# Kernel optimization log

Measured on AMD Instinct MI355X. Metric: run time of the kernel, lower is better.

Reference implementation:

```python
import jax, jax.numpy as jnp
import numpy as np

B, S, IN, E, H, NH = 32, 1024, 16, 128, 256, 4
DH = E // NH
EPS = 1e-5


def _ln(x, g, b):
    mu = jnp.mean(x, axis=-1, keepdims=True)
    var = jnp.mean(jnp.square(x - mu), axis=-1, keepdims=True)
    return (x - mu) * jax.lax.rsqrt(var + EPS) * g + b


def setup_inputs() -> dict:
    key = jax.random.key(0)
    ks = iter(jax.random.split(key, 32))
    n = lambda shape, s=0.02: jax.random.normal(next(ks), shape, jnp.float32) * s
    inp = {
        "x": jax.random.normal(next(ks), (B, S, IN), jnp.float32),
        "mask": jax.random.uniform(next(ks), (B, S), jnp.float32),
        "embed_w": n((E, IN)), "embed_b": jnp.zeros((E,), jnp.float32),
        # 3 encoder layers, params stacked on leading layer axis
        "in_proj_w": n((3, 3 * E, E)), "in_proj_b": jnp.zeros((3, 3 * E), jnp.float32),
        "out_w": n((3, E, E)), "out_b": jnp.zeros((3, E), jnp.float32),
        "ln1_g": jnp.ones((3, E), jnp.float32), "ln1_b": jnp.zeros((3, E), jnp.float32),
        "ln2_g": jnp.ones((3, E), jnp.float32), "ln2_b": jnp.zeros((3, E), jnp.float32),
        "ffn_w1": n((3, E, E)), "ffn_b1": jnp.zeros((3, E), jnp.float32),
        "ffn_w2": n((3, E, E)), "ffn_b2": jnp.zeros((3, E), jnp.float32),
        "cls_w1": n((H, E)), "cls_b1": jnp.zeros((H,), jnp.float32),
        "cls_w2": n((H, H)), "cls_b2": jnp.zeros((H,), jnp.float32),
        "cls_w3": n((H, H)), "cls_b3": jnp.zeros((H,), jnp.float32),
        "cls_w4": n((1, H)), "cls_b4": jnp.zeros((1,), jnp.float32),
    }
    return inp


def _encoder_layer(x, ipw, ipb, ow, ob, g1, b1, g2, b2, w1, fb1, w2, fb2):
    # PyTorch TransformerEncoderLayer, norm_first=False (post-norm), relu FFN
    qkv = x @ ipw.T + ipb                      # [B,S,3E]
    q, k, v = jnp.split(qkv, 3, axis=-1)
    q = q.reshape(B, S, NH, DH).transpose(0, 2, 1, 3)
    k = k.reshape(B, S, NH, DH).transpose(0, 2, 1, 3)
    v = v.reshape(B, S, NH, DH).transpose(0, 2, 1, 3)
    scores = jnp.einsum("bhqd,bhkd->bhqk", q, k) / np.sqrt(DH)  # naive O(S^2) math SDPA
    attn = jax.nn.softmax(scores, axis=-1)
    o = jnp.einsum("bhqk,bhkd->bhqd", attn, v)
    o = o.transpose(0, 2, 1, 3).reshape(B, S, E) @ ow.T + ob
    x = _ln(x + o, g1, b1)
    ff = jax.nn.relu(x @ w1.T + fb1) @ w2.T + fb2
    return _ln(x + ff, g2, b2)


def reference(x, mask, embed_w, embed_b, in_proj_w, in_proj_b, out_w, out_b,
              ln1_g, ln1_b, ln2_g, ln2_b, ffn_w1, ffn_b1, ffn_w2, ffn_b2,
              cls_w1, cls_b1, cls_w2, cls_b2, cls_w3, cls_b3, cls_w4, cls_b4):
    h = jax.nn.relu(x @ embed_w.T + embed_b)   # [B,S,E]
    for i in range(3):
        h = _encoder_layer(h, in_proj_w[i], in_proj_b[i], out_w[i], out_b[i],
                           ln1_g[i], ln1_b[i], ln2_g[i], ln2_b[i],
                           ffn_w1[i], ffn_b1[i], ffn_w2[i], ffn_b2[i])
    pooled = jnp.sum(h * mask[:, :, None], axis=1)  # [B,E] masked sum pool
    z = jax.nn.relu(pooled @ cls_w1.T + cls_b1)
    z = jax.nn.relu(z @ cls_w2.T + cls_b2)
    z = jax.nn.relu(z @ cls_w3.T + cls_b3)
    return jax.nn.sigmoid(z @ cls_w4.T + cls_b4)    # [B,1]
```

## Files before the change

kernel.cpp:

```cpp
#include <hip/hip_runtime.h>
#include <hip/hip_bf16.h>
#include <math.h>

#define B 32
#define S 1024
#define IN_DIM 16
#define E 128
#define NH 4
#define DH 32
#define HDIM 256
#define ROWS (B*S)
#define EPS 1e-5f

#define N_IPW (3*384*128)
#define N_SQ  (3*128*128)
#define NCVT ((N_IPW + 3*N_SQ) / 256)

typedef __bf16 bf16x8 __attribute__((ext_vector_type(8)));
typedef __bf16 bf16x4 __attribute__((ext_vector_type(4)));
typedef __bf16 bf16x2 __attribute__((ext_vector_type(2)));
typedef float f32x4 __attribute__((ext_vector_type(4)));

union BF2U { bf16x2 b; unsigned int u; };
__device__ inline unsigned int pk2(float a, float b) {
    BF2U x; x.b[0] = (__bf16)a; x.b[1] = (__bf16)b; return x.u;
}

union U8 { bf16x8 v8; bf16x4 v4[2]; };
__device__ inline void st8(__bf16* p, bf16x8 v) {
    U8 u; u.v8 = v;
    *(bf16x4*)p = u.v4[0];
    *(bf16x4*)(p + 4) = u.v4[1];
}
__device__ inline bf16x8 ld8(const __bf16* p) {
    U8 u;
    u.v4[0] = *(const bf16x4*)p;
    u.v4[1] = *(const bf16x4*)(p + 4);
    return u.v8;
}

__global__ __launch_bounds__(256) void k_embedcvt(
        const float* __restrict__ ipw, const float* __restrict__ ow,
        const float* __restrict__ w1, const float* __restrict__ w2,
        __bf16* __restrict__ wbo,
        const float* __restrict__ x, const float* __restrict__ W,
        const float* __restrict__ bias, __bf16* __restrict__ hb)
{
    int t = threadIdx.x;
    if (blockIdx.x < NCVT) {
        int i = blockIdx.x * 256 + t;
        float v;
        if (i < N_IPW) v = ipw[i];
        else if (i < N_IPW + N_SQ) v = ow[i - N_IPW];
        else if (i < N_IPW + 2 * N_SQ) v = w1[i - N_IPW - N_SQ];
        else v = w2[i - N_IPW - 2 * N_SQ];
        wbo[i] = (__bf16)v;
        return;
    }
    int row0 = (blockIdx.x - NCVT) * 16;
    __shared__ float xs[16][16];
    xs[t >> 4][t & 15] = x[(row0 + (t >> 4)) * IN_DIM + (t & 15)];
    __syncthreads();
    int sub = t >> 7, tc = t & 127;
    float w[16];
#pragma unroll
    for (int i = 0; i < 16; ++i) w[i] = W[tc * 16 + i];
    float bb = bias[tc];
#pragma unroll
    for (int rr = 0; rr < 8; ++rr) {
        int lr = sub * 8 + rr;
        float acc = bb;
#pragma unroll
        for (int i = 0; i < 16; ++i) acc += xs[lr][i] * w[i];
        hb[(size_t)(row0 + lr) * E + tc] = (__bf16)fmaxf(acc, 0.f);
    }
}

__global__ __launch_bounds__(256) void k_gemm_qkv(const __bf16* __restrict__ A,
        const __bf16* __restrict__ W, const float* __restrict__ bias,
        __bf16* __restrict__ qk, __bf16* __restrict__ vt)
{
    __shared__ __attribute__((aligned(16))) __bf16 As[128][132];
    __shared__ __attribute__((aligned(16))) __bf16 Ws[64][132];
    int t = threadIdx.x;
    int m0 = blockIdx.y * 128, n0 = blockIdx.x * 64;
    {
        int arow = t >> 1, acol = (t & 1) * 64;
        const __bf16* Ap = A + (size_t)(m0 + arow) * 128 + acol;
#pragma unroll
        for (int j = 0; j < 8; ++j)
            st8(&As[arow][acol + j * 8], *(const bf16x8*)&Ap[j * 8]);
        int wrow = t >> 2, wcol = (t & 3) * 32;
        const __bf16* Wp = W + (size_t)(n0 + wrow) * 128 + wcol;
#pragma unroll
        for (int j = 0; j < 4; ++j)
            st8(&Ws[wrow][wcol + j * 8], *(const bf16x8*)&Wp[j * 8]);
    }
    __syncthreads();
    int lane = t & 63, wv = t >> 6;
    int l15 = lane & 15, quad = lane >> 4;
    int wm = (wv & 1) * 64, wn = (wv >> 1) * 32;
    f32x4 acc[2][4];
#pragma unroll
    for (int i = 0; i < 2; ++i)
#pragma unroll
        for (int j = 0; j < 4; ++j) acc[i][j] = (f32x4){0.f, 0.f, 0.f, 0.f};
#pragma unroll
    for (int kc = 0; kc < 4; ++kc) {
        bf16x8 aw[2], ba[4];
#pragma unroll
        for (int nc = 0; nc < 2; ++nc)
            aw[nc] = ld8(&Ws[wn + nc * 16 + l15][kc * 32 + quad * 8]);
#pragma unroll
        for (int mc = 0; mc < 4; ++mc)
            ba[mc] = ld8(&As[wm + mc * 16 + l15][kc * 32 + quad * 8]);
#pragma unroll
        for (int nc = 0; nc < 2; ++nc)
#pragma unroll
            for (int mc = 0; mc < 4; ++mc)
                acc[nc][mc] = __builtin_amdgcn_mfma_f32_16x16x32_bf16(aw[nc], ba[mc], acc[nc][mc], 0, 0, 0);
    }
#pragma unroll
    for (int nc = 0; nc < 2; ++nc) {
        float4 bv = *(const float4*)&bias[n0 + wn + nc * 16 + quad * 4];
#pragma unroll
        for (int mc = 0; mc < 4; ++mc) {
            float v0 = acc[nc][mc][0] + bv.x;
            float v1 = acc[nc][mc][1] + bv.y;
            float v2 = acc[nc][mc][2] + bv.z;
            float v3 = acc[nc][mc][3] + bv.w;
            int n = n0 + wn + nc * 16 + quad * 4;
            int m = m0 + wm + mc * 16 + l15;
            if (n < 256) {
                uint2 u; u.x = pk2(v0, v1); u.y = pk2(v2, v3);
                *(uint2*)&qk[(size_t)m * 256 + n] = u;
            } else {
                int dp = n - 256;
                int hq = dp >> 5, d0 = dp & 31;
                __bf16* vp = vt + (((size_t)(m >> 10) * 4 + hq) * 32 + d0) * 1024 + (m & 1023);
                vp[0] = (__bf16)v0; vp[1024] = (__bf16)v1;
                vp[2048] = (__bf16)v2; vp[3072] = (__bf16)v3;
            }
        }
    }
}

__global__ __launch_bounds__(256) void k_attn4(const __bf16* __restrict__ qk,
        const __bf16* __restrict__ vt, __bf16* __restrict__ O)
{
    int qt = blockIdx.x & 7, bh = blockIdx.x >> 3;
    int hh = bh & 3, b = bh >> 2;
    __shared__ __attribute__((aligned(16))) __bf16 Kb[2][64][36];
    __shared__ __attribute__((aligned(16))) __bf16 Vb[2][32][68];
    __shared__ __attribute__((aligned(16))) __bf16 Pm[2][4][16][68];
    int t = threadIdx.x, lane = t & 63, wv = t >> 6;
    int l15 = lane & 15, quad = lane >> 4;
    const __bf16* qbase = qk + (size_t)(b * S) * 256 + hh * 32;
    const __bf16* kbase = qk + (size_t)(b * S) * 256 + 128 + hh * 32;
    const __bf16* vbase = vt + ((size_t)(b * 4 + hh) * 32) * 1024;
    const float qscale = 0.1767766952966369f * 1.4426950408889634f * 8388608.0f;
    const float C2 = 1065101558.0f;
    const f32x4 cinit = {C2, C2, C2, C2};
    bf16x8 vones;
#pragma unroll
    for (int j = 0; j < 8; ++j) vones[j] = (__bf16)1.0f;

    bf16x8 bQ[2];
#pragma unroll
    for (int gq = 0; gq < 2; ++gq) {
        bf16x8 qv = *(const bf16x8*)&qbase[(size_t)(qt * 128 + gq * 64 + wv * 16 + l15) * 256 + quad * 8];
#pragma unroll
        for (int j = 0; j < 8; ++j) bQ[gq][j] = (__bf16)((float)qv[j] * qscale);
    }

    int ksr = t >> 2, ksc = (t & 3) * 8;
    int vsr = t >> 3, vsc = (t & 7) * 8;

    {
        bf16x8 k0 = *(const bf16x8*)&kbase[(size_t)ksr * 256 + ksc];
        bf16x8 v0 = *(const bf16x8*)&vbase[(size_t)vsr * 1024 + vsc];
        st8(&Kb[0][ksr][ksc], k0);
        st8(&Vb[0][vsr][vsc], v0);
    }
    __syncthreads();

    f32x4 o[2][2], ol[2];
#pragma unroll
    for (int gq = 0; gq < 2; ++gq) {
        ol[gq] = (f32x4){0.f, 0.f, 0.f, 0.f};
#pragma unroll
        for (int j = 0; j < 2; ++j) o[gq][j] = (f32x4){0.f, 0.f, 0.f, 0.f};
    }

    for (int it = 0; it < 16; ++it) {
        const int cur = it & 1;
        bf16x8 knext, vnext;
        if (it < 15) {
            knext = *(const bf16x8*)&kbase[(size_t)((it + 1) * 64 + ksr) * 256 + ksc];
            vnext = *(const bf16x8*)&vbase[(size_t)vsr * 1024 + (it + 1) * 64 + vsc];
        }
        bf16x8 aK[4];
#pragma unroll
        for (int c = 0; c < 4; ++c)
            aK[c] = ld8(&Kb[cur][c * 16 + l15][quad * 8]);
        bf16x8 bv[2][2];
#pragma unroll
        for (int kc = 0; kc < 2; ++kc) {
            bv[kc][0] = ld8(&Vb[cur][l15][kc * 32 + quad * 8]);
            bv[kc][1] = ld8(&Vb[cur][16 + l15][kc * 32 + quad * 8]);
        }
#pragma unroll
        for (int gq = 0; gq < 2; ++gq) {
            f32x4 sf[4];
#pragma unroll
            for (int c = 0; c < 4; ++c)
                sf[c] = __builtin_amdgcn_mfma_f32_16x16x32_bf16(aK[c], bQ[gq], cinit, 0, 0, 0);
#pragma unroll
            for (int c = 0; c < 4; ++c) {
                int i0 = (int)sf[c][0];
                int i1 = (int)sf[c][1];
                int i2 = (int)sf[c][2];
                int i3 = (int)sf[c][3];
                uint2 u;
                u.x = __builtin_amdgcn_perm((unsigned)i1, (unsigned)i0, 0x07060302u);
                u.y = __builtin_amdgcn_perm((unsigned)i3, (unsigned)i2, 0x07060302u);
                *(uint2*)&Pm[gq][wv][l15][c * 16 + quad * 4] = u;
            }
        }
        __asm__ __volatile__("" ::: "memory");
#pragma unroll
        for (int gq = 0; gq < 2; ++gq) {
#pragma unroll
            for (int kc = 0; kc < 2; ++kc) {
                bf16x8 ap = ld8(&Pm[gq][wv][l15][kc * 32 + quad * 8]);
                o[gq][0] = __builtin_amdgcn_mfma_f32_16x16x32_bf16(ap, bv[kc][0], o[gq][0], 0, 0, 0);
                o[gq][1] = __builtin_amdgcn_mfma_f32_16x16x32_bf16(ap, bv[kc][1], o[gq][1], 0, 0, 0);
                ol[gq]   = __builtin_amdgcn_mfma_f32_16x16x32_bf16(ap, vones, ol[gq], 0, 0, 0);
            }
        }
        __asm__ __volatile__("" ::: "memory");
        if (it < 15) {
            st8(&Kb[cur ^ 1][ksr][ksc], knext);
            st8(&Vb[cur ^ 1][vsr][vsc], vnext);
            __syncthreads();
        }
    }

#pragma unroll
    for (int gq = 0; gq < 2; ++gq) {
#pragma unroll
        for (int reg = 0; reg < 4; ++reg) {
            float linv = 1.f / ol[gq][reg];
            int row = qt * 128 + gq * 64 + wv * 16 + quad * 4 + reg;
            __bf16* op = O + ((size_t)(b * S) + row) * E + hh * 32;
            op[l15] = (__bf16)(o[gq][0][reg] * linv);
            op[16 + l15] = (__bf16)(o[gq][1][reg] * linv);
        }
    }
}

__global__ __launch_bounds__(256) void k_layer2(const __bf16* __restrict__ t0b,
        const __bf16* __restrict__ Wo, const float* __restrict__ ob,
        const float* __restrict__ g1, const float* __restrict__ bt1,
        const __bf16* __restrict__ W1, const float* __restrict__ b1v,
        const __bf16* __restrict__ W2, const float* __restrict__ b2v,
        const float* __restrict__ g2, const float* __restrict__ bt2,
        __bf16* __restrict__ hb)
{
    __shared__ __attribute__((aligned(16))) __bf16 As[64][132];
    __shared__ __attribute__((aligned(16))) __bf16 Ws[128][132];
    __shared__ float red[2][64][2];
    int t = threadIdx.x;
    int m0 = blockIdx.x * 64;
    int arow = t >> 2, acol = (t & 3) * 32;
    int wrow = t >> 1, wcol = (t & 1) * 64;
    {
        const __bf16* Ap = t0b + (size_t)(m0 + arow) * 128 + acol;
#pragma unroll
        for (int j = 0; j < 4; ++j)
            st8(&As[arow][acol + j * 8], *(const bf16x8*)&Ap[j * 8]);
        const __bf16* Wp = Wo + (size_t)wrow * 128 + wcol;
#pragma unroll
        for (int j = 0; j < 8; ++j)
            st8(&Ws[wrow][wcol + j * 8], *(const bf16x8*)&Wp[j * 8]);
    }
    __syncthreads();
    int lane = t & 63, wv = t >> 6;
    int l15 = lane & 15, quad = lane >> 4;
    int nh = wv & 1, mh = wv >> 1;
    f32x4 acc[4][2];

#pragma unroll
    for (int i = 0; i < 4; ++i)
#pragma unroll
        for (int j = 0; j < 2; ++j) acc[i][j] = (f32x4){0.f, 0.f, 0.f, 0.f};
#pragma unroll
    for (int kc = 0; kc < 4; ++kc) {
        bf16x8 aw[4], ba[2];
#pragma unroll
        for (int nc = 0; nc < 4; ++nc)
            aw[nc] = ld8(&Ws[nh * 64 + nc * 16 + l15][kc * 32 + quad * 8]);
#pragma unroll
        for (int mc = 0; mc < 2; ++mc)
            ba[mc] = ld8(&As[mh * 32 + mc * 16 + l15][kc * 32 + quad * 8]);
#pragma unroll
        for (int nc = 0; nc < 4; ++nc)
#pragma unroll
            for (int mc = 0; mc < 2; ++mc)
                acc[nc][mc] = __builtin_amdgcn_mfma_f32_16x16x32_bf16(aw[nc], ba[mc], acc[nc][mc], 0, 0, 0);
    }
    float s1[2] = {0.f, 0.f}, s2[2] = {0.f, 0.f};
#pragma unroll
    for (int nc = 0; nc < 4; ++nc) {
        float4 bv = *(const float4*)&ob[nh * 64 + nc * 16 + quad * 4];
#pragma unroll
        for (int mc = 0; mc < 2; ++mc) {
            int m = m0 + mh * 32 + mc * 16 + l15;
            bf16x4 rv = *(const bf16x4*)&hb[(size_t)m * 128 + nh * 64 + nc * 16 + quad * 4];
            acc[nc][mc][0] += bv.x + (float)rv[0];
            acc[nc][mc][1] += bv.y + (float)rv[1];
            acc[nc][mc][2] += bv.z + (float)rv[2];
            acc[nc][mc][3] += bv.w + (float)rv[3];
#pragma unroll
            for (int i = 0; i < 4; ++i) {
                s1[mc] += acc[nc][mc][i];
                s2[mc] += acc[nc][mc][i] * acc[nc][mc][i];
            }
        }
    }
#pragma unroll
    for (int mc = 0; mc < 2; ++mc) {
        s1[mc] += __shfl_xor(s1[mc], 16); s1[mc] += __shfl_xor(s1[mc], 32);
        s2[mc] += __shfl_xor(s2[mc], 16); s2[mc] += __shfl_xor(s2[mc], 32);
    }
    if (quad == 0) {
#pragma unroll
        for (int mc = 0; mc < 2; ++mc) {
            red[nh][mh * 32 + mc * 16 + l15][0] = s1[mc];
            red[nh][mh * 32 + mc * 16 + l15][1] = s2[mc];
        }
    }
    __syncthreads();
    float mu[2], rs[2];
#pragma unroll
    for (int mc = 0; mc < 2; ++mc) {
        int r = mh * 32 + mc * 16 + l15;
        float S1 = red[0][r][0] + red[1][r][0];
        float S2 = red[0][r][1] + red[1][r][1];
        mu[mc] = S1 * (1.f / 128.f);
        float var = S2 * (1.f / 128.f) - mu[mc] * mu[mc];
        rs[mc] = rsqrtf(var + EPS);
    }
    bf16x4 res2[4][2];
#pragma unroll
    for (int nc = 0; nc < 4; ++nc) {
        float4 gv = *(const float4*)&g1[nh * 64 + nc * 16 + quad * 4];
        float4 bb = *(const float4*)&bt1[nh * 64 + nc * 16 + quad * 4];
#pragma unroll
        for (int mc = 0; mc < 2; ++mc) {
            float o0 = (acc[nc][mc][0] - mu[mc]) * rs[mc] * gv.x + bb.x;
            float o1 = (acc[nc][mc][1] - mu[mc]) * rs[mc] * gv.y + bb.y;
            float o2 = (acc[nc][mc][2] - mu[mc]) * rs[mc] * gv.z + bb.z;
            float o3 = (acc[nc][mc][3] - mu[mc]) * rs[mc] * gv.w + bb.w;
            bf16x4 xb;
            xb[0] = (__bf16)o0; xb[1] = (__bf16)o1;
            xb[2] = (__bf16)o2; xb[3] = (__bf16)o3;
            res2[nc][mc] = xb;
            *(bf16x4*)&As[mh * 32 + mc * 16 + l15][nh * 64 + nc * 16 + quad * 4] = xb;
        }
    }
    {
        const __bf16* Wp = W1 + (size_t)wrow * 128 + wcol;
#pragma unroll
        for (int j = 0; j < 8; ++j)
            st8(&Ws[wrow][wcol + j * 8], *(const bf16x8*)&Wp[j * 8]);
    }
    __syncthreads();

#pragma unroll
    for (int i = 0; i < 4; ++i)
#pragma unroll
        for (int j = 0; j < 2; ++j) acc[i][j] = (f32x4){0.f, 0.f, 0.f, 0.f};
#pragma unroll
    for (int kc = 0; kc < 4; ++kc) {
        bf16x8 aw[4], ba[2];
#pragma unroll
        for (int nc = 0; nc < 4; ++nc)
            aw[nc] = ld8(&Ws[nh * 64 + nc * 16 + l15][kc * 32 + quad * 8]);
#pragma unroll
        for (int mc = 0; mc < 2; ++mc)
            ba[mc] = ld8(&As[mh * 32 + mc * 16 + l15][kc * 32 + quad * 8]);
#pragma unroll
        for (int nc = 0; nc < 4; ++nc)
#pragma unroll
            for (int mc = 0; mc < 2; ++mc)
                acc[nc][mc] = __builtin_amdgcn_mfma_f32_16x16x32_bf16(aw[nc], ba[mc], acc[nc][mc], 0, 0, 0);
    }
    __syncthreads();
#pragma unroll
    for (int nc = 0; nc < 4; ++nc) {
        float4 bv = *(const float4*)&b1v[nh * 64 + nc * 16 + quad * 4];
#pragma unroll
        for (int mc = 0; mc < 2; ++mc) {
            float v0 = fmaxf(acc[nc][mc][0] + bv.x, 0.f);
            float v1 = fmaxf(acc[nc][mc][1] + bv.y, 0.f);
            float v2 = fmaxf(acc[nc][mc][2] + bv.z, 0.f);
            float v3 = fmaxf(acc[nc][mc][3] + bv.w, 0.f);
            uint2 u; u.x = pk2(v0, v1); u.y = pk2(v2, v3);
            *(uint2*)&As[mh * 32 + mc * 16 + l15][nh * 64 + nc * 16 + quad * 4] = u;
        }
    }
    {
        const __bf16* Wp = W2 + (size_t)wrow * 128 + wcol;
#pragma unroll
        for (int j = 0; j < 8; ++j)
            st8(&Ws[wrow][wcol + j * 8], *(const bf16x8*)&Wp[j * 8]);
    }
    __syncthreads();

#pragma unroll
    for (int i = 0; i < 4; ++i)
#pragma unroll
        for (int j = 0; j < 2; ++j) acc[i][j] = (f32x4){0.f, 0.f, 0.f, 0.f};
#pragma unroll
    for (int kc = 0; kc < 4; ++kc) {
        bf16x8 aw[4], ba[2];
#pragma unroll
        for (int nc = 0; nc < 4; ++nc)
            aw[nc] = ld8(&Ws[nh * 64 + nc * 16 + l15][kc * 32 + quad * 8]);
#pragma unroll
        for (int mc = 0; mc < 2; ++mc)
            ba[mc] = ld8(&As[mh * 32 + mc * 16 + l15][kc * 32 + quad * 8]);
#pragma unroll
        for (int nc = 0; nc < 4; ++nc)
#pragma unroll
            for (int mc = 0; mc < 2; ++mc)
                acc[nc][mc] = __builtin_amdgcn_mfma_f32_16x16x32_bf16(aw[nc], ba[mc], acc[nc][mc], 0, 0, 0);
    }
    s1[0] = s1[1] = s2[0] = s2[1] = 0.f;
#pragma unroll
    for (int nc = 0; nc < 4; ++nc) {
        float4 bv = *(const float4*)&b2v[nh * 64 + nc * 16 + quad * 4];
#pragma unroll
        for (int mc = 0; mc < 2; ++mc) {
            acc[nc][mc][0] += bv.x + (float)res2[nc][mc][0];
            acc[nc][mc][1] += bv.y + (float)res2[nc][mc][1];
            acc[nc][mc][2] += bv.z + (float)res2[nc][mc][2];
            acc[nc][mc][3] += bv.w + (float)res2[nc][mc][3];
#pragma unroll
            for (int i = 0; i < 4; ++i) {
                s1[mc] += acc[nc][mc][i];
                s2[mc] += acc[nc][mc][i] * acc[nc][mc][i];
            }
        }
    }
#pragma unroll
    for (int mc = 0; mc < 2; ++mc) {
        s1[mc] += __shfl_xor(s1[mc], 16); s1[mc] += __shfl_xor(s1[mc], 32);
        s2[mc] += __shfl_xor(s2[mc], 16); s2[mc] += __shfl_xor(s2[mc], 32);
    }
    if (quad == 0) {
#pragma unroll
        for (int mc = 0; mc < 2; ++mc) {
            red[nh][mh * 32 + mc * 16 + l15][0] = s1[mc];
            red[nh][mh * 32 + mc * 16 + l15][1] = s2[mc];
        }
    }
    __syncthreads();
#pragma unroll
    for (int mc = 0; mc < 2; ++mc) {
        int r = mh * 32 + mc * 16 + l15;
        float S1 = red[0][r][0] + red[1][r][0];
        float S2 = red[0][r][1] + red[1][r][1];
        mu[mc] = S1 * (1.f / 128.f);
        float var = S2 * (1.f / 128.f) - mu[mc] * mu[mc];
        rs[mc] = rsqrtf(var + EPS);
    }
#pragma unroll
    for (int nc = 0; nc < 4; ++nc) {
        float4 gv = *(const float4*)&g2[nh * 64 + nc * 16 + quad * 4];
        float4 bb = *(const float4*)&bt2[nh * 64 + nc * 16 + quad * 4];
#pragma unroll
        for (int mc = 0; mc < 2; ++mc) {
            int m = m0 + mh * 32 + mc * 16 + l15;
            float o0 = (acc[nc][mc][0] - mu[mc]) * rs[mc] * gv.x + bb.x;
            float o1 = (acc[nc][mc][1] - mu[mc]) * rs[mc] * gv.y + bb.y;
            float o2 = (acc[nc][mc][2] - mu[mc]) * rs[mc] * gv.z + bb.z;
            float o3 = (acc[nc][mc][3] - mu[mc]) * rs[mc] * gv.w + bb.w;
            uint2 u; u.x = pk2(o0, o1); u.y = pk2(o2, o3);
            *(uint2*)&hb[(size_t)m * 128 + nh * 64 + nc * 16 + quad * 4] = u;
        }
    }
}

__global__ __launch_bounds__(128) void k_pool1(const __bf16* __restrict__ h,
        const float* __restrict__ mask, float* __restrict__ part)
{
    int bx = blockIdx.x;
    int b = bx >> 3, ch = bx & 7, t = threadIdx.x;
    float acc = 0.f;
    const __bf16* hp = h + (size_t)(b * S + ch * 128) * E + t;
    const float* mp = mask + b * S + ch * 128;
    for (int s = 0; s < 128; ++s) acc += (float)hp[(size_t)s * E] * mp[s];
    part[(size_t)bx * E + t] = acc;
}

__global__ __launch_bounds__(256) void k_head(const float* __restrict__ part,
        const float* __restrict__ cw1, const float* __restrict__ cb1,
        const float* __restrict__ cw2, const float* __restrict__ cb2,
        const float* __restrict__ cw3, const float* __restrict__ cb3,
        const float* __restrict__ cw4, const float* __restrict__ cb4,
        float* __restrict__ out)
{
    int b = blockIdx.x, t = threadIdx.x;
    __shared__ float p[128], za[256], zb[256];
    __shared__ float red4[4];
    if (t < 128) {
        float a = 0.f;
#pragma unroll
        for (int c = 0; c < 8; ++c) a += part[(size_t)(b * 8 + c) * 128 + t];
        p[t] = a;
    }
    __syncthreads();
    float a1 = cb1[t];
    for (int k = 0; k < 128; ++k) a1 += p[k] * cw1[t * 128 + k];
    za[t] = fmaxf(a1, 0.f);
    __syncthreads();
    float a2 = cb2[t];
    for (int k = 0; k < 256; ++k) a2 += za[k] * cw2[t * 256 + k];
    zb[t] = fmaxf(a2, 0.f);
    __syncthreads();
    float a3 = cb3[t];
    for (int k = 0; k < 256; ++k) a3 += zb[k] * cw3[t * 256 + k];
    float z3 = fmaxf(a3, 0.f);
    float prt = z3 * cw4[t];
#pragma unroll
    for (int o2 = 32; o2; o2 >>= 1) prt += __shfl_xor(prt, o2);
    if ((t & 63) == 0) red4[t >> 6] = prt;
    __syncthreads();
    if (t == 0) {
        float sum = red4[0] + red4[1] + red4[2] + red4[3] + cb4[0];
        out[b] = 1.f / (1.f + __expf(-sum));
    }
}

extern "C" void kernel_launch(void* const* d_in, const int* in_sizes, int n_in,
                              void* d_out, int out_size, void* d_ws, size_t ws_size,
                              hipStream_t stream)
{
    const float* x     = (const float*)d_in[0];
    const float* mask  = (const float*)d_in[1];
    const float* emb_w = (const float*)d_in[2];
    const float* emb_b = (const float*)d_in[3];
    const float* ipw   = (const float*)d_in[4];
    const float* ipb   = (const float*)d_in[5];
    const float* ow    = (const float*)d_in[6];
    const float* ob    = (const float*)d_in[7];
    const float* ln1g  = (const float*)d_in[8];
    const float* ln1b  = (const float*)d_in[9];
    const float* ln2g  = (const float*)d_in[10];
    const float* ln2b  = (const float*)d_in[11];
    const float* w1    = (const float*)d_in[12];
    const float* fb1   = (const float*)d_in[13];
    const float* w2    = (const float*)d_in[14];
    const float* fb2   = (const float*)d_in[15];
    const float* cw1   = (const float*)d_in[16];
    const float* cb1   = (const float*)d_in[17];
    const float* cw2   = (const float*)d_in[18];
    const float* cb2   = (const float*)d_in[19];
    const float* cw3   = (const float*)d_in[20];
    const float* cb3   = (const float*)d_in[21];
    const float* cw4   = (const float*)d_in[22];
    const float* cb4   = (const float*)d_in[23];

    char* p = (char*)d_ws;
    __bf16* hb   = (__bf16*)p;   p += (size_t)ROWS * E * 2;
    __bf16* qkb  = (__bf16*)p;   p += (size_t)ROWS * 256 * 2;
    __bf16* vtb  = (__bf16*)p;   p += (size_t)ROWS * 32 * 4 * 2 / 4;
    __bf16* t0b  = (__bf16*)p;   p += (size_t)ROWS * E * 2;
    __bf16* wb   = (__bf16*)p;   p += (size_t)(N_IPW + 3 * N_SQ) * 2;
    float* part  = (float*)p;    p += (size_t)B * 8 * E * 4;

    __bf16* wb_ipw = wb;
    __bf16* wb_ow  = wb + N_IPW;
    __bf16* wb_w1  = wb_ow + N_SQ;
    __bf16* wb_w2  = wb_w1 + N_SQ;

    k_embedcvt<<<NCVT + ROWS / 16, 256, 0, stream>>>(
        ipw, ow, w1, w2, wb, x, emb_w, emb_b, hb);
    for (int L = 0; L < 3; ++L) {
        k_gemm_qkv<<<dim3(6, ROWS / 128), 256, 0, stream>>>(
            hb, wb_ipw + (size_t)L * 384 * 128, ipb + L * 384, qkb, vtb);
        k_attn4<<<B * NH * (S / 128), 256, 0, stream>>>(qkb, vtb, t0b);
        k_layer2<<<ROWS / 64, 256, 0, stream>>>(
            t0b, wb_ow + (size_t)L * 128 * 128, ob + L * 128,
            ln1g + L * E, ln1b + L * E,
            wb_w1 + (size_t)L * 128 * 128, fb1 + L * 128,
            wb_w2 + (size_t)L * 128 * 128, fb2 + L * 128,
            ln2g + L * E, ln2b + L * E, hb);
    }
    k_pool1<<<B * 8, 128, 0, stream>>>(hb, mask, part);
    k_head<<<B, 256, 0, stream>>>(part, cw1, cb1, cw2, cb2, cw3, cb3, cw4, cb4,
                                  (float*)d_out);
}
```

Before: 333.7 us.

## Fuse QKV projection into attention kernel with full-sequence K/V in LDS

```diff
diff --git a/kernel.cpp b/kernel.cpp
--- a/kernel.cpp
+++ b/kernel.cpp
@@ -20,6 +20,8 @@
 typedef __bf16 bf16x4 __attribute__((ext_vector_type(4)));
 typedef __bf16 bf16x2 __attribute__((ext_vector_type(2)));
 typedef float f32x4 __attribute__((ext_vector_type(4)));
+
+#define MFMA16 __builtin_amdgcn_mfma_f32_16x16x32_bf16
 
 union BF2U { bf16x2 b; unsigned int u; };
 __device__ inline unsigned int pk2(float a, float b) {
@@ -76,187 +78,168 @@
     }
 }
 
-__global__ __launch_bounds__(256) void k_gemm_qkv(const __bf16* __restrict__ A,
-        const __bf16* __restrict__ W, const float* __restrict__ bias,
-        __bf16* __restrict__ qk, __bf16* __restrict__ vt)
+__global__ __launch_bounds__(512, 2) void k_qkvattn(
+        const __bf16* __restrict__ hb, const __bf16* __restrict__ Wip,
+        const float* __restrict__ bip, __bf16* __restrict__ O)
 {
-    __shared__ __attribute__((aligned(16))) __bf16 As[128][132];
-    __shared__ __attribute__((aligned(16))) __bf16 Ws[64][132];
-    int t = threadIdx.x;
-    int m0 = blockIdx.y * 128, n0 = blockIdx.x * 64;
-    {
-        int arow = t >> 1, acol = (t & 1) * 64;
-        const __bf16* Ap = A + (size_t)(m0 + arow) * 128 + acol;
-#pragma unroll
-        for (int j = 0; j < 8; ++j)
-            st8(&As[arow][acol + j * 8], *(const bf16x8*)&Ap[j * 8]);
-        int wrow = t >> 2, wcol = (t & 3) * 32;
-        const __bf16* Wp = W + (size_t)(n0 + wrow) * 128 + wcol;
-#pragma unroll
-        for (int j = 0; j < 4; ++j)
-            st8(&Ws[wrow][wcol + j * 8], *(const bf16x8*)&Wp[j * 8]);
-    }
-    __syncthreads();
-    int lane = t & 63, wv = t >> 6;
-    int l15 = lane & 15, quad = lane >> 4;
-    int wm = (wv & 1) * 64, wn = (wv >> 1) * 32;
-    f32x4 acc[2][4];
-#pragma unroll
-    for (int i = 0; i < 2; ++i)
-#pragma unroll
-        for (int j = 0; j < 4; ++j) acc[i][j] = (f32x4){0.f, 0.f, 0.f, 0.f};
-#pragma unroll
-    for (int kc = 0; kc < 4; ++kc) {
-        bf16x8 aw[2], ba[4];
-#pragma unroll
-        for (int nc = 0; nc < 2; ++nc)
-            aw[nc] = ld8(&Ws[wn + nc * 16 + l15][kc * 32 + quad * 8]);
-#pragma unroll
-        for (int mc = 0; mc < 4; ++mc)
-            ba[mc] = ld8(&As[wm + mc * 16 + l15][kc * 32 + quad * 8]);
-#pragma unroll
-        for (int nc = 0; nc < 2; ++nc)
-#pragma unroll
-            for (int mc = 0; mc < 4; ++mc)
-                acc[nc][mc] = __builtin_amdgcn_mfma_f32_16x16x32_bf16(aw[nc], ba[mc], acc[nc][mc], 0, 0, 0);
-    }
-#pragma unroll
-    for (int nc = 0; nc < 2; ++nc) {
-        float4 bv = *(const float4*)&bias[n0 + wn + nc * 16 + quad * 4];
-#pragma unroll
-        for (int mc = 0; mc < 4; ++mc) {
-            float v0 = acc[nc][mc][0] + bv.x;
-            float v1 = acc[nc][mc][1] + bv.y;
-            float v2 = acc[nc][mc][2] + bv.z;
-            float v3 = acc[nc][mc][3] + bv.w;
-            int n = n0 + wn + nc * 16 + quad * 4;
-            int m = m0 + wm + mc * 16 + l15;
-            if (n < 256) {
-                uint2 u; u.x = pk2(v0, v1); u.y = pk2(v2, v3);
-                *(uint2*)&qk[(size_t)m * 256 + n] = u;
-            } else {
-                int dp = n - 256;
-                int hq = dp >> 5, d0 = dp & 31;
-                __bf16* vp = vt + (((size_t)(m >> 10) * 4 + hq) * 32 + d0) * 1024 + (m & 1023);
-                vp[0] = (__bf16)v0; vp[1024] = (__bf16)v1;
-                vp[2048] = (__bf16)v2; vp[3072] = (__bf16)v3;
-            }
-        }
-    }
-}
-
-__global__ __launch_bounds__(256) void k_attn4(const __bf16* __restrict__ qk,
-        const __bf16* __restrict__ vt, __bf16* __restrict__ O)
-{
-    int qt = blockIdx.x & 7, bh = blockIdx.x >> 3;
-    int hh = bh & 3, b = bh >> 2;
-    __shared__ __attribute__((aligned(16))) __bf16 Kb[2][64][36];
-    __shared__ __attribute__((aligned(16))) __bf16 Vb[2][32][68];
-    __shared__ __attribute__((aligned(16))) __bf16 Pm[2][4][16][68];
+    __shared__ __attribute__((aligned(16))) __bf16 Ksh[1024][36];
+    __shared__ __attribute__((aligned(16))) __bf16 Vsh[32][1036];
+    __shared__ __attribute__((aligned(16))) __bf16 Pm[8][16][68];
+
     int t = threadIdx.x, lane = t & 63, wv = t >> 6;
     int l15 = lane & 15, quad = lane >> 4;
-    const __bf16* qbase = qk + (size_t)(b * S) * 256 + hh * 32;
-    const __bf16* kbase = qk + (size_t)(b * S) * 256 + 128 + hh * 32;
-    const __bf16* vbase = vt + ((size_t)(b * 4 + hh) * 32) * 1024;
+    int lb = ((blockIdx.x & 7) << 5) | (blockIdx.x >> 3);
+    int half = lb & 1, bh = lb >> 1;
+    int hh = bh & 3, b = bh >> 2;
+
+    const __bf16* hpanel = hb + (size_t)b * S * E;
+
     const float qscale = 0.1767766952966369f * 1.4426950408889634f * 8388608.0f;
     const float C2 = 1065101558.0f;
     const f32x4 cinit = {C2, C2, C2, C2};
+    const f32x4 z4 = {0.f, 0.f, 0.f, 0.f};
+
+    bf16x8 bWk[2][4], bWv[2][4];
+#pragma unroll
+    for (int df = 0; df < 2; ++df)
+#pragma unroll
+        for (int kc = 0; kc < 4; ++kc) {
+            bWk[df][kc] = *(const bf16x8*)&Wip[(size_t)(128 + hh*32 + df*16 + l15)*128 + kc*32 + quad*8];
+            bWv[df][kc] = *(const bf16x8*)&Wip[(size_t)(256 + hh*32 + df*16 + l15)*128 + kc*32 + quad*8];
+        }
+    float bk0 = bip[128 + hh*32 + l15],      bk1 = bip[128 + hh*32 + 16 + l15];
+    float bvb0 = bip[256 + hh*32 + l15],     bvb1 = bip[256 + hh*32 + 16 + l15];
+
+    int qrow0 = half*512 + wv*64;
+    bf16x8 bQ[4];
+    {
+        bf16x8 bWq[2][4];
+#pragma unroll
+        for (int df = 0; df < 2; ++df)
+#pragma unroll
+            for (int kc = 0; kc < 4; ++kc)
+                bWq[df][kc] = *(const bf16x8*)&Wip[(size_t)(hh*32 + df*16 + l15)*128 + kc*32 + quad*8];
+        float bq0 = bip[hh*32 + l15], bq1 = bip[hh*32 + 16 + l15];
+#pragma unroll
+        for (int qf = 0; qf < 4; ++qf) {
+            bf16x8 af[4];
+#pragma unroll
+            for (int kc = 0; kc < 4; ++kc)
+                af[kc] = *(const bf16x8*)&hpanel[(size_t)(qrow0 + qf*16 + l15)*128 + kc*32 + quad*8];
+            f32x4 a0 = z4, a1 = z4;
+#pragma unroll
+            for (int kc = 0; kc < 4; ++kc) {
+                a0 = MFMA16(af[kc], bWq[0][kc], a0, 0, 0, 0);
+                a1 = MFMA16(af[kc], bWq[1][kc], a1, 0, 0, 0);
+            }
+#pragma unroll
+            for (int r = 0; r < 4; ++r) {
+                Pm[wv][quad*4 + r][l15]      = (__bf16)((a0[r] + bq0) * qscale);
+                Pm[wv][quad*4 + r][16 + l15] = (__bf16)((a1[r] + bq1) * qscale);
+            }
+            __asm__ __volatile__("" ::: "memory");
+            bQ[qf] = ld8(&Pm[wv][l15][quad*8]);
+            __asm__ __volatile__("" ::: "memory");
+        }
+    }
+
+    {
+        int srow = wv*16 + l15;
+        bf16x8 af[4], ag[4];
+#pragma unroll
+        for (int kc = 0; kc < 4; ++kc)
+            af[kc] = *(const bf16x8*)&hpanel[(size_t)srow*128 + kc*32 + quad*8];
+        for (int c = 0; c < 8; ++c) {
+            if (c < 7) {
+#pragma unroll
+                for (int kc = 0; kc < 4; ++kc)
+                    ag[kc] = *(const bf16x8*)&hpanel[(size_t)((c+1)*128 + srow)*128 + kc*32 + quad*8];
+            }
+            f32x4 k0 = z4, k1 = z4, v0 = z4, v1 = z4;
+#pragma unroll
+            for (int kc = 0; kc < 4; ++kc) {
+                k0 = MFMA16(af[kc], bWk[0][kc], k0, 0, 0, 0);
+                k1 = MFMA16(af[kc], bWk[1][kc], k1, 0, 0, 0);
+                v0 = MFMA16(af[kc], bWv[0][kc], v0, 0, 0, 0);
+                v1 = MFMA16(af[kc], bWv[1][kc], v1, 0, 0, 0);
+            }
+            int s0 = c*128 + wv*16 + quad*4;
+#pragma unroll
+            for (int r = 0; r < 4; ++r) {
+                Ksh[s0 + r][l15]      = (__bf16)(k0[r] + bk0);
+                Ksh[s0 + r][16 + l15] = (__bf16)(k1[r] + bk1);
+            }
+            uint2 u0, u1;
+            u0.x = pk2(v0[0] + bvb0, v0[1] + bvb0);
+            u0.y = pk2(v0[2] + bvb0, v0[3] + bvb0);
+            u1.x = pk2(v1[0] + bvb1, v1[1] + bvb1);
+            u1.y = pk2(v1[2] + bvb1, v1[3] + bvb1);
+            *(uint2*)&Vsh[l15][s0] = u0;
+            *(uint2*)&Vsh[16 + l15][s0] = u1;
+#pragma unroll
+            for (int kc = 0; kc < 4; ++kc) af[kc] = ag[kc];
+        }
+    }
+    __syncthreads();
+
     bf16x8 vones;
 #pragma unroll
     for (int j = 0; j < 8; ++j) vones[j] = (__bf16)1.0f;
-
-    bf16x8 bQ[2];
-#pragma unroll
-    for (int gq = 0; gq < 2; ++gq) {
-        bf16x8 qv = *(const bf16x8*)&qbase[(size_t)(qt * 128 + gq * 64 + wv * 16 + l15) * 256 + quad * 8];
-#pragma unroll
-        for (int j = 0; j < 8; ++j) bQ[gq][j] = (__bf16)((float)qv[j] * qscale);
-    }
-
-    int ksr = t >> 2, ksc = (t & 3) * 8;
-    int vsr = t >> 3, vsc = (t & 7) * 8;
-
-    {
-        bf16x8 k0 = *(const bf16x8*)&kbase[(size_t)ksr * 256 + ksc];
-        bf16x8 v0 = *(const bf16x8*)&vbase[(size_t)vsr * 1024 + vsc];
-        st8(&Kb[0][ksr][ksc], k0);
-        st8(&Vb[0][vsr][vsc], v0);
-    }
-    __syncthreads();
-
-    f32x4 o[2][2], ol[2];
-#pragma unroll
-    for (int gq = 0; gq < 2; ++gq) {
-        ol[gq] = (f32x4){0.f, 0.f, 0.f, 0.f};
-#pragma unroll
-        for (int j = 0; j < 2; ++j) o[gq][j] = (f32x4){0.f, 0.f, 0.f, 0.f};
-    }
-
-    for (int it = 0; it < 16; ++it) {
-        const int cur = it & 1;
-        bf16x8 knext, vnext;
-        if (it < 15) {
-            knext = *(const bf16x8*)&kbase[(size_t)((it + 1) * 64 + ksr) * 256 + ksc];
-            vnext = *(const bf16x8*)&vbase[(size_t)vsr * 1024 + (it + 1) * 64 + vsc];
-        }
-        bf16x8 aK[4];
-#pragma unroll
-        for (int c = 0; c < 4; ++c)
-            aK[c] = ld8(&Kb[cur][c * 16 + l15][quad * 8]);
-        bf16x8 bv[2][2];
+    f32x4 o[4][2], ol[4];
+#pragma unroll
+    for (int qf = 0; qf < 4; ++qf) {
+        ol[qf] = z4; o[qf][0] = z4; o[qf][1] = z4;
+    }
+
+    for (int c = 0; c < 16; ++c) {
+        bf16x8 aK[4], bV[2][2];
+#pragma unroll
+        for (int ck = 0; ck < 4; ++ck)
+            aK[ck] = ld8(&Ksh[c*64 + ck*16 + l15][quad*8]);
 #pragma unroll
         for (int kc = 0; kc < 2; ++kc) {
-            bv[kc][0] = ld8(&Vb[cur][l15][kc * 32 + quad * 8]);
-            bv[kc][1] = ld8(&Vb[cur][16 + l15][kc * 32 + quad * 8]);
-        }
-#pragma unroll
-        for (int gq = 0; gq < 2; ++gq) {
+            bV[kc][0] = ld8(&Vsh[l15][c*64 + kc*32 + quad*8]);
+            bV[kc][1] = ld8(&Vsh[16 + l15][c*64 + kc*32 + quad*8]);
+        }
+#pragma unroll
+        for (int qf = 0; qf < 4; ++qf) {
             f32x4 sf[4];
 #pragma unroll
-            for (int c = 0; c < 4; ++c)
-                sf[c] = __builtin_amdgcn_mfma_f32_16x16x32_bf16(aK[c], bQ[gq], cinit, 0, 0, 0);
-#pragma unroll
-            for (int c = 0; c < 4; ++c) {
-                int i0 = (int)sf[c][0];
-                int i1 = (int)sf[c][1];
-                int i2 = (int)sf[c][2];
-                int i3 = (int)sf[c][3];
+            for (int ck = 0; ck < 4; ++ck)
+                sf[ck] = MFMA16(aK[ck], bQ[qf], cinit, 0, 0, 0);
+#pragma unroll
+            for (int ck = 0; ck < 4; ++ck) {
+                int i0 = (int)sf[ck][0];
+                int i1 = (int)sf[ck][1];
+                int i2 = (int)sf[ck][2];
+                int i3 = (int)sf[ck][3];
                 uint2 u;
                 u.x = __builtin_amdgcn_perm((unsigned)i1, (unsigned)i0, 0x07060302u);
                 u.y = __builtin_amdgcn_perm((unsigned)i3, (unsigned)i2, 0x07060302u);
-                *(uint2*)&Pm[gq][wv][l15][c * 16 + quad * 4] = u;
-            }
-        }
-        __asm__ __volatile__("" ::: "memory");
-#pragma unroll
-        for (int gq = 0; gq < 2; ++gq) {
+                *(uint2*)&Pm[wv][l15][ck*16 + quad*4] = u;
+            }
+            __asm__ __volatile__("" ::: "memory");
 #pragma unroll
             for (int kc = 0; kc < 2; ++kc) {
-                bf16x8 ap = ld8(&Pm[gq][wv][l15][kc * 32 + quad * 8]);
-                o[gq][0] = __builtin_amdgcn_mfma_f32_16x16x32_bf16(ap, bv[kc][0], o[gq][0], 0, 0, 0);
-                o[gq][1] = __builtin_amdgcn_mfma_f32_16x16x32_bf16(ap, bv[kc][1], o[gq][1], 0, 0, 0);
-                ol[gq]   = __builtin_amdgcn_mfma_f32_16x16x32_bf16(ap, vones, ol[gq], 0, 0, 0);
-            }
-        }
-        __asm__ __volatile__("" ::: "memory");
-        if (it < 15) {
-            st8(&Kb[cur ^ 1][ksr][ksc], knext);
-            st8(&Vb[cur ^ 1][vsr][vsc], vnext);
-            __syncthreads();
-        }
-    }
-
-#pragma unroll
-    for (int gq = 0; gq < 2; ++gq) {
-#pragma unroll
-        for (int reg = 0; reg < 4; ++reg) {
-            float linv = 1.f / ol[gq][reg];
-            int row = qt * 128 + gq * 64 + wv * 16 + quad * 4 + reg;
-            __bf16* op = O + ((size_t)(b * S) + row) * E + hh * 32;
-            op[l15] = (__bf16)(o[gq][0][reg] * linv);
-            op[16 + l15] = (__bf16)(o[gq][1][reg] * linv);
-        }
-    }
+                bf16x8 ap = ld8(&Pm[wv][l15][kc*32 + quad*8]);
+                o[qf][0] = MFMA16(ap, bV[kc][0], o[qf][0], 0, 0, 0);
+                o[qf][1] = MFMA16(ap, bV[kc][1], o[qf][1], 0, 0, 0);
+                ol[qf]   = MFMA16(ap, vones, ol[qf], 0, 0, 0);
+            }
+            __asm__ __volatile__("" ::: "memory");
+        }
+    }
+
+#pragma unroll
+    for (int qf = 0; qf < 4; ++qf)
+#pragma unroll
+        for (int r = 0; r < 4; ++r) {
+            float linv = 1.f / ol[qf][r];
+            int row = half*512 + wv*64 + qf*16 + quad*4 + r;
+            __bf16* op = O + ((size_t)(b * S) + row) * E + hh*32;
+            op[l15]      = (__bf16)(o[qf][0][r] * linv);
+            op[16 + l15] = (__bf16)(o[qf][1][r] * linv);
+        }
 }
 
 __global__ __launch_bounds__(256) void k_layer2(const __bf16* __restrict__ t0b,
@@ -307,7 +290,7 @@
         for (int nc = 0; nc < 4; ++nc)
 #pragma unroll
             for (int mc = 0; mc < 2; ++mc)
-                acc[nc][mc] = __builtin_amdgcn_mfma_f32_16x16x32_bf16(aw[nc], ba[mc], acc[nc][mc], 0, 0, 0);
+                acc[nc][mc] = MFMA16(aw[nc], ba[mc], acc[nc][mc], 0, 0, 0);
     }
     float s1[2] = {0.f, 0.f}, s2[2] = {0.f, 0.f};
 #pragma unroll
@@ -394,7 +377,7 @@
         for (int nc = 0; nc < 4; ++nc)
 #pragma unroll
             for (int mc = 0; mc < 2; ++mc)
-                acc[nc][mc] = __builtin_amdgcn_mfma_f32_16x16x32_bf16(aw[nc], ba[mc], acc[nc][mc], 0, 0, 0);
+                acc[nc][mc] = MFMA16(aw[nc], ba[mc], acc[nc][mc], 0, 0, 0);
     }
     __syncthreads();
 #pragma unroll
@@ -435,7 +418,7 @@
         for (int nc = 0; nc < 4; ++nc)
 #pragma unroll
             for (int mc = 0; mc < 2; ++mc)
-                acc[nc][mc] = __builtin_amdgcn_mfma_f32_16x16x32_bf16(aw[nc], ba[mc], acc[nc][mc], 0, 0, 0);
+                acc[nc][mc] = MFMA16(aw[nc], ba[mc], acc[nc][mc], 0, 0, 0);
     }
     s1[0] = s1[1] = s2[0] = s2[1] = 0.f;
 #pragma unroll
@@ -575,8 +558,8 @@
 
     char* p = (char*)d_ws;
     __bf16* hb   = (__bf16*)p;   p += (size_t)ROWS * E * 2;
-    __bf16* qkb  = (__bf16*)p;   p += (size_t)ROWS * 256 * 2;
-    __bf16* vtb  = (__bf16*)p;   p += (size_t)ROWS * 32 * 4 * 2 / 4;
+    p += (size_t)ROWS * 256 * 2;
+    p += (size_t)ROWS * 32 * 4 * 2 / 4;
     __bf16* t0b  = (__bf16*)p;   p += (size_t)ROWS * E * 2;
     __bf16* wb   = (__bf16*)p;   p += (size_t)(N_IPW + 3 * N_SQ) * 2;
     float* part  = (float*)p;    p += (size_t)B * 8 * E * 4;
@@ -589,9 +572,8 @@
     k_embedcvt<<<NCVT + ROWS / 16, 256, 0, stream>>>(
         ipw, ow, w1, w2, wb, x, emb_w, emb_b, hb);
     for (int L = 0; L < 3; ++L) {
-        k_gemm_qkv<<<dim3(6, ROWS / 128), 256, 0, stream>>>(
-            hb, wb_ipw + (size_t)L * 384 * 128, ipb + L * 384, qkb, vtb);
-        k_attn4<<<B * NH * (S / 128), 256, 0, stream>>>(qkb, vtb, t0b);
+        k_qkvattn<<<B * NH * 2, 512, 0, stream>>>(
+            hb, wb_ipw + (size_t)L * 384 * 128, ipb + L * 384, t0b);
         k_layer2<<<ROWS / 64, 256, 0, stream>>>(
             t0b, wb_ow + (size_t)L * 128 * 128, ob + L * 128,
             ln1g + L * E, ln1b + L * E,
```

Result: faster. 309.9 us (-7.1%).
